# Performance work log

Measured on AMD Instinct MI355X. Metric: run time of the kernel, lower is better.

The kernel has to match this reference:

```python
import jax, jax.numpy as jnp
import numpy as np

V = 32000      # vocab
TMAX = 1024    # BLOCK_SIZE
D = 768        # N_EMBD
H = 12         # N_HEAD
L = 12         # N_LAYER
HS = D // H    # head_size
FF = 4 * D
B, T = 4, 1024


def setup_inputs() -> dict:
    key = jax.random.key(0)
    ks = iter(jax.random.split(key, 40))
    n = lambda shape: 0.02 * jax.random.normal(next(ks), shape, dtype=jnp.float32)
    return dict(
        idx=jax.random.randint(next(ks), (B, T), 0, V),
        targets=jax.random.randint(next(ks), (B, T), 0, V),
        tok_emb=n((V, D)),
        pos_emb=n((TMAX, D)),
        Wq=n((L, H, D, HS)), Wk=n((L, H, D, HS)), Wv=n((L, H, D, HS)),
        Wo=n((L, D, D)), bo=jnp.zeros((L, D)),
        W1=n((L, D, FF)), b1=jnp.zeros((L, FF)),
        W2=n((L, FF, D)), b2=jnp.zeros((L, D)),
        ln1_g=jnp.ones((L, D)), ln1_b=jnp.zeros((L, D)),
        ln2_g=jnp.ones((L, D)), ln2_b=jnp.zeros((L, D)),
        lnf_g=jnp.ones((D,)), lnf_b=jnp.zeros((D,)),
        Wlm=n((D, V)), blm=jnp.zeros((V,)),
    )


def _ln(x, g, b, eps=1e-5):
    m = x.mean(-1, keepdims=True)
    v = x.var(-1, keepdims=True)
    return (x - m) * jax.lax.rsqrt(v + eps) * g + b


def reference(idx, targets, tok_emb, pos_emb, Wq, Wk, Wv, Wo, bo,
              W1, b1, W2, b2, ln1_g, ln1_b, ln2_g, ln2_b, lnf_g, lnf_b,
              Wlm, blm):
    Bsz, Tt = idx.shape
    x = tok_emb[idx] + pos_emb[:Tt]                      # [B,T,D]
    causal = jnp.tril(jnp.ones((Tt, Tt), dtype=bool))     # [T,T]

    def layer(x, p):
        wq, wk, wv, wo, bob, w1, b1b, w2, b2b, g1, be1, g2, be2 = p
        h = _ln(x, g1, be1)
        q = jnp.einsum('btd,hdk->bhtk', h, wq)
        k = jnp.einsum('btd,hdk->bhtk', h, wk)
        v = jnp.einsum('btd,hdk->bhtk', h, wv)
        wei = jnp.einsum('bhtk,bhsk->bhts', q, k) * (HS ** -0.5)
        wei = jnp.where(causal, wei, -jnp.inf)
        wei = jax.nn.softmax(wei, axis=-1)                # dropout=0 in eval
        att = jnp.einsum('bhts,bhsk->bhtk', wei, v)
        att = att.transpose(0, 2, 1, 3).reshape(Bsz, Tt, H * HS)  # concat heads
        x = x + att @ wo + bob
        h2 = _ln(x, g2, be2)
        x = x + jax.nn.relu(h2 @ w1 + b1b) @ w2 + b2b
        return x, None

    x, _ = jax.lax.scan(layer, x,
                        (Wq, Wk, Wv, Wo, bo, W1, b1, W2, b2,
                         ln1_g, ln1_b, ln2_g, ln2_b))
    x = _ln(x, lnf_g, lnf_b)
    logits = x @ Wlm + blm                                # [B,T,V]
    lf = logits.reshape(Bsz * Tt, V)
    tf = targets.reshape(-1)
    logp = jax.nn.log_softmax(lf, axis=-1)
    loss = -jnp.take_along_axis(logp, tf[:, None], axis=1).mean()
    return lf, loss
```

## Files before the change

kernel.cpp:

```cpp
#include <hip/hip_runtime.h>

constexpr int C_B   = 4;
constexpr int C_T   = 1024;
constexpr int C_D   = 768;
constexpr int C_H   = 12;
constexpr int C_HS  = 64;
constexpr int C_FF  = 3072;
constexpr int C_V   = 32000;
constexpr int C_L   = 12;
constexpr int ROWS  = C_B * C_T;
constexpr int QKVN  = 3 * C_D;
constexpr int NCB   = C_V / 256;

typedef __bf16 bf16;
typedef __attribute__((ext_vector_type(8))) __bf16 bf16x8;
typedef __attribute__((ext_vector_type(4))) float  f32x4;
typedef __attribute__((ext_vector_type(4))) short  s16x4;

static __device__ __forceinline__ void gload16(const void* g, void* l) {
  __builtin_amdgcn_global_load_lds((const __attribute__((address_space(1))) void*)g,
                                   (__attribute__((address_space(3))) void*)l,
                                   16, 0, 0);
}

__global__ __launch_bounds__(256) void embed_kernel(const int* __restrict__ idx,
    const float* __restrict__ tok, const float* __restrict__ pos, float* __restrict__ x) {
  int gid = blockIdx.x * 256 + threadIdx.x;
  int row = gid / C_D, d = gid - row * C_D;
  int t = row & (C_T - 1);
  x[gid] = tok[(long)idx[row] * C_D + d] + pos[(long)t * C_D + d];
}

__global__ __launch_bounds__(256) void ln_kernel(const float* __restrict__ x,
    const float* __restrict__ g, const float* __restrict__ bb, long goff,
    bf16* __restrict__ out) {
  int row = blockIdx.x, tid = threadIdx.x;
  const float* xr = x + (long)row * C_D;
  float v0 = xr[tid], v1 = xr[tid + 256], v2 = xr[tid + 512];
  float s = v0 + v1 + v2;
  float s2 = v0 * v0 + v1 * v1 + v2 * v2;
#pragma unroll
  for (int off = 32; off > 0; off >>= 1) {
    s  += __shfl_down(s, off);
    s2 += __shfl_down(s2, off);
  }
  __shared__ float sm[4], sq[4];
  if ((tid & 63) == 0) { sm[tid >> 6] = s; sq[tid >> 6] = s2; }
  __syncthreads();
  s  = sm[0] + sm[1] + sm[2] + sm[3];
  s2 = sq[0] + sq[1] + sq[2] + sq[3];
  float mean = s * (1.f / C_D);
  float var  = s2 * (1.f / C_D) - mean * mean;
  float rstd = rsqrtf(var + 1e-5f);
  bf16* orow = out + (long)row * C_D;
  orow[tid]       = (bf16)((v0 - mean) * rstd * g[goff + tid]       + bb[goff + tid]);
  orow[tid + 256] = (bf16)((v1 - mean) * rstd * g[goff + tid + 256] + bb[goff + tid + 256]);
  orow[tid + 512] = (bf16)((v2 - mean) * rstd * g[goff + tid + 512] + bb[goff + tid + 512]);
}

__global__ __launch_bounds__(256) void transpose_all_kernel(
    const float* __restrict__ Wq, const float* __restrict__ Wk,
    const float* __restrict__ Wv, const float* __restrict__ Wo,
    const float* __restrict__ W1, const float* __restrict__ W2,
    const float* __restrict__ Wlm,
    bf16* __restrict__ wqkvt, bf16* __restrict__ wot,
    bf16* __restrict__ w1t, bf16* __restrict__ w2t, bf16* __restrict__ wlmt) {
  int bid = blockIdx.x;
  const float* src; bf16* dst; int K, N, ntn, t;
  if (bid < 82944) {
    int l = bid / 6912, sub = bid % 6912;
    if (sub < 1728) {
      int which = sub / 576, r = sub % 576, head = r / 48;
      t = r % 48;
      const float* W = which == 0 ? Wq : which == 1 ? Wk : Wv;
      src = W + (long)l * C_H * C_D * C_HS + (long)head * C_D * C_HS;
      dst = wqkvt + (long)l * QKVN * C_D + (long)which * C_D * C_D + (long)head * C_HS * C_D;
      K = C_D; N = C_HS; ntn = 2;
    } else if (sub < 2304) {
      t = sub - 1728;
      src = Wo + (long)l * C_D * C_D;  dst = wot + (long)l * C_D * C_D;
      K = C_D; N = C_D; ntn = 24;
    } else if (sub < 4608) {
      t = sub - 2304;
      src = W1 + (long)l * C_D * C_FF; dst = w1t + (long)l * C_FF * C_D;
      K = C_D; N = C_FF; ntn = 96;
    } else {
      t = sub - 4608;
      src = W2 + (long)l * C_FF * C_D; dst = w2t + (long)l * C_D * C_FF;
      K = C_FF; N = C_D; ntn = 24;
    }
  } else {
    t = bid - 82944; src = Wlm; dst = wlmt;
    K = C_D; N = C_V; ntn = C_V / 32;
  }
  __shared__ bf16 tile[32][33];
  int tn = t % ntn, tk = t / ntn;
  int c = threadIdx.x & 31, r = threadIdx.x >> 5;
#pragma unroll
  for (int it = 0; it < 4; ++it)
    tile[r + 8 * it][c] = (bf16)src[(long)(tk * 32 + r + 8 * it) * N + tn * 32 + c];
  __syncthreads();
#pragma unroll
  for (int it = 0; it < 4; ++it)
    dst[(long)(tn * 32 + r + 8 * it) * K + tk * 32 + c] = tile[c][r + 8 * it];
}

template <int MODE>
__global__ __launch_bounds__(512) void gemm256(const bf16* __restrict__ A,
    const bf16* __restrict__ Bt, const float* __restrict__ bias, long boff,
    void* __restrict__ outp, float* __restrict__ lossp, int N, int K) {
  __shared__ __attribute__((aligned(16))) char smem[131072];
  int tid = threadIdx.x;
  int l = tid & 63, w = tid >> 6;
  int wm = w >> 2, wn = w & 3;
  int lg = l >> 4, lr = l & 15;

  int nwg = gridDim.x;
  int fid = blockIdx.x;
  int swz = (fid & 7) * (nwg >> 3) + (fid >> 3);
  long row0 = (long)(swz & 15) * 256;
  long col0 = (long)(swz >> 4) * 256;
  int cbi = (int)(col0 >> 8);

  int Y0 = tid * 16, Y1 = 8192 + tid * 16;
  auto dec = [](int Y, int& R, int& C) {
    int s = Y >> 10, y = Y & 1023;
    int r15 = y >> 6, z = y & 63;
    int q = (z ^ ((r15 & 8) << 2)) >> 4;
    R = (s >> 1) * 16 + r15;
    C = (s & 1) * 32 + q * 8;
  };
  int R0, C0, R1, C1;
  dec(Y0, R0, C0);  dec(Y1, R1, C1);
  const bf16* Ab = A  + row0 * K;
  const bf16* Bb = Bt + col0 * K;

  auto stage = [&](int d, int kt) {
    char* bb = smem + d * 65536;
    long kc = (long)kt * 64;
    gload16(Ab + (long)R0 * K + kc + C0, bb + Y0);
    gload16(Ab + (long)R1 * K + kc + C1, bb + Y1);
    gload16(Ab + (long)(128 + R0) * K + kc + C0, bb + 16384 + Y0);
    gload16(Ab + (long)(128 + R1) * K + kc + C1, bb + 16384 + Y1);
    gload16(Bb + (long)R0 * K + kc + C0, bb + 32768 + Y0);
    gload16(Bb + (long)R1 * K + kc + C1, bb + 32768 + Y1);
    gload16(Bb + (long)(128 + R0) * K + kc + C0, bb + 49152 + Y0);
    gload16(Bb + (long)(128 + R1) * K + kc + C1, bb + 49152 + Y1);
  };

  f32x4 acc[8][4];
  const f32x4 fz = {0.f, 0.f, 0.f, 0.f};
#pragma unroll
  for (int mf = 0; mf < 8; ++mf)
#pragma unroll
    for (int nf = 0; nf < 4; ++nf) acc[mf][nf] = fz;

  int aoff = lr * 64 + ((lg * 16) ^ ((lr & 8) << 2));
  int nk = K >> 6;
  stage(0, 0);
  int d = 0;
  for (int kt = 0; kt < nk; ++kt) {
    __syncthreads();
    if (kt + 1 < nk) stage(d ^ 1, kt + 1);
    const char* aB = smem + d * 65536 + wm * 16384;
    const char* bB = smem + d * 65536 + 32768 + (wn >> 1) * 16384;
    bf16x8 bfrag[4][2];
#pragma unroll
    for (int nf = 0; nf < 4; ++nf)
#pragma unroll
      for (int k = 0; k < 2; ++k)
        bfrag[nf][k] = *(const bf16x8*)(bB + ((((wn & 1) * 4 + nf) * 2 + k) << 10) + aoff);
#pragma unroll
    for (int p = 0; p < 4; ++p) {
      bf16x8 af[2][2];
#pragma unroll
      for (int mi = 0; mi < 2; ++mi)
#pragma unroll
        for (int k = 0; k < 2; ++k)
          af[mi][k] = *(const bf16x8*)(aB + (((p * 2 + mi) * 2 + k) << 10) + aoff);
      __builtin_amdgcn_s_setprio(1);
#pragma unroll
      for (int mi = 0; mi < 2; ++mi)
#pragma unroll
        for (int nf = 0; nf < 4; ++nf)
#pragma unroll
          for (int k = 0; k < 2; ++k)
            acc[p * 2 + mi][nf] = __builtin_amdgcn_mfma_f32_16x16x32_bf16(
                af[mi][k], bfrag[nf][k], acc[p * 2 + mi][nf], 0, 0, 0);
      __builtin_amdgcn_s_setprio(0);
    }
    d ^= 1;
  }
  __syncthreads();

  if (MODE == 0 || MODE == 1) {
    bf16* lc = (bf16*)smem;
#pragma unroll
    for (int nf = 0; nf < 4; ++nf) {
      int col = wn * 64 + nf * 16 + lr;
      float bv = bias ? bias[boff + col0 + col] : 0.f;
#pragma unroll
      for (int mf = 0; mf < 8; ++mf) {
        int rb = wm * 128 + mf * 16 + lg * 4;
#pragma unroll
        for (int r = 0; r < 4; ++r) {
          float v = acc[mf][nf][r] + bv;
          if (MODE == 1) v = fmaxf(v, 0.f);
          lc[(rb + r) * 256 + col] = (bf16)v;
        }
      }
    }
    __syncthreads();
#pragma unroll
    for (int it = 0; it < 16; ++it) {
      int byte = it * 8192 + tid * 16;
      int rl = byte >> 9, cb = byte & 511;
      *(bf16x8*)((bf16*)outp + (row0 + rl) * N + col0 + (cb >> 1)) =
          *(const bf16x8*)(smem + byte);
    }
  } else {
#pragma unroll
    for (int h = 0; h < 2; ++h) {
      if (h) __syncthreads();
      if (wm == h) {
        float* lf = (float*)smem;
#pragma unroll
        for (int nf = 0; nf < 4; ++nf) {
          int col = wn * 64 + nf * 16 + lr;
          float bv = bias ? bias[boff + col0 + col] : 0.f;
#pragma unroll
          for (int mf = 0; mf < 8; ++mf) {
            int rb = mf * 16 + lg * 4;
#pragma unroll
            for (int r = 0; r < 4; ++r)
              lf[(rb + r) * 256 + col] = acc[mf][nf][r] + bv;
          }
        }
      }
      __syncthreads();
#pragma unroll
      for (int it = 0; it < 16; ++it) {
        int byte = it * 8192 + tid * 16;
        int rl = byte >> 10, cb = byte & 1023;
        *(f32x4*)((float*)outp + (row0 + h * 128 + rl) * N + col0 + (cb >> 2)) =
            *(const f32x4*)(smem + byte);
      }
      if (MODE == 3 && lossp) {
        const float* lf = (const float*)smem;
        int row = tid >> 2, chunk = tid & 3;
        float M = -1e30f, S = 0.f;
#pragma unroll
        for (int j = 0; j < 16; ++j) {
          int jj = (j + row) & 15;
          f32x4 v = *(const f32x4*)(lf + row * 256 + chunk * 64 + jj * 4);
#pragma unroll
          for (int q = 0; q < 4; ++q) {
            float xv = v[q];
            if (xv > M) { S *= __expf(M - xv); M = xv; }
            S += __expf(xv - M);
          }
        }
#pragma unroll
        for (int off = 1; off < 4; off <<= 1) {
          float Mo = __shfl_xor(M, off), So = __shfl_xor(S, off);
          float Mn = fmaxf(M, Mo);
          S = S * __expf(M - Mn) + So * __expf(Mo - Mn);
          M = Mn;
        }
        if (chunk == 0) {
          long pi = ((row0 + h * 128 + row) * NCB + cbi) * 2;
          lossp[pi] = M;  lossp[pi + 1] = S;
        }
      }
    }
  }
}

template <int MODE>
__global__ __launch_bounds__(256) void gemm_bt(const bf16* __restrict__ A,
    const bf16* __restrict__ Bt, const float* __restrict__ bias, long boff,
    void* __restrict__ outp, float* __restrict__ resid, int N, int K) {
  __shared__ __attribute__((aligned(16))) char smem[32768];
  int tid = threadIdx.x;
  int l = tid & 63;
  int w = tid >> 6, wr = w >> 1, wc = w & 1;
  int lg = l >> 4, lr = l & 15;

  int nwg = gridDim.x;
  int fid = blockIdx.x;
  int swz = (fid & 7) * (nwg >> 3) + (fid >> 3);
  long row0 = (long)(swz & 31) * 128;
  long col0 = (long)(swz >> 5) * 128;

  const bf16* ga = A  + (row0 + (tid >> 2)) * K + (tid & 3) * 8;
  const bf16* gb = Bt + (col0 + (tid >> 2)) * K + (tid & 3) * 8;

  f32x4 acc[4][4];
  const f32x4 fz = {0.f, 0.f, 0.f, 0.f};
#pragma unroll
  for (int m = 0; m < 4; ++m)
#pragma unroll
    for (int n = 0; n < 4; ++n) acc[m][n] = fz;

  int nk = K >> 5;
  {
    bf16* la = (bf16*)smem + tid * 8;
    bf16* lb = (bf16*)(smem + 8192) + tid * 8;
    gload16(ga, la);  gload16(ga + (long)64 * K, la + 2048);
    gload16(gb, lb);  gload16(gb + (long)64 * K, lb + 2048);
    ga += 32; gb += 32;
  }
  int cur = 0;
  for (int t = 0; t < nk; ++t) {
    __syncthreads();
    if (t + 1 < nk) {
      char* bufb = smem + (cur ^ 1) * 16384;
      bf16* la = (bf16*)bufb + tid * 8;
      bf16* lb = (bf16*)(bufb + 8192) + tid * 8;
      gload16(ga, la);  gload16(ga + (long)64 * K, la + 2048);
      gload16(gb, lb);  gload16(gb + (long)64 * K, lb + 2048);
      ga += 32; gb += 32;
    }
    const bf16* cA = (const bf16*)(smem + cur * 16384);
    const bf16* cB = (const bf16*)(smem + cur * 16384 + 8192);
    bf16x8 af[4], bfr[4];
#pragma unroll
    for (int m = 0; m < 4; ++m)
      af[m] = *(const bf16x8*)(cA + (wr * 64 + m * 16 + lr) * 32 + lg * 8);
#pragma unroll
    for (int n = 0; n < 4; ++n)
      bfr[n] = *(const bf16x8*)(cB + (wc * 64 + n * 16 + lr) * 32 + lg * 8);
#pragma unroll
    for (int m = 0; m < 4; ++m)
#pragma unroll
      for (int n = 0; n < 4; ++n)
        acc[m][n] = __builtin_amdgcn_mfma_f32_16x16x32_bf16(af[m], bfr[n], acc[m][n], 0, 0, 0);
    cur ^= 1;
  }
  __syncthreads();

  if (MODE == 0 || MODE == 1) {
    bf16* lc = (bf16*)smem;
#pragma unroll
    for (int n = 0; n < 4; ++n) {
      int gcl = wc * 64 + n * 16 + lr;
      float bv = bias ? bias[boff + col0 + gcl] : 0.f;
#pragma unroll
      for (int m = 0; m < 4; ++m) {
        int rb = wr * 64 + m * 16 + lg * 4;
#pragma unroll
        for (int r = 0; r < 4; ++r) {
          float v = acc[m][n][r] + bv;
          if (MODE == 1) v = fmaxf(v, 0.f);
          lc[(rb + r) * 128 + gcl] = (bf16)v;
        }
      }
    }
    __syncthreads();
#pragma unroll
    for (int it = 0; it < 8; ++it) {
      int byte = it * 4096 + tid * 16;
      int rl = byte >> 8;
      int cb = byte & 255;
      *(bf16x8*)((bf16*)outp + (row0 + rl) * N + col0 + (cb >> 1)) =
          *(const bf16x8*)(smem + byte);
    }
  } else {
#pragma unroll
    for (int pair = 0; pair < 2; ++pair) {
      float* lcf = (float*)smem;
#pragma unroll
      for (int n = 0; n < 4; ++n) {
        int gcl = wc * 64 + n * 16 + lr;
        float bv = bias ? bias[boff + col0 + gcl] : 0.f;
#pragma unroll
        for (int mi = 0; mi < 2; ++mi) {
          int m = pair * 2 + mi;
          int rl = wr * 32 + mi * 16 + lg * 4;
#pragma unroll
          for (int r = 0; r < 4; ++r)
            lcf[(rl + r) * 128 + gcl] = acc[m][n][r] + bv;
        }
      }
      __syncthreads();
#pragma unroll
      for (int it = 0; it < 8; ++it) {
        int byte = it * 4096 + tid * 16;
        int rl = byte >> 9;
        int cb = byte & 511;
        long gr = row0 + (rl >> 5) * 64 + pair * 32 + ((rl >> 4) & 1) * 16 + (rl & 15);
        f32x4 v = *(const f32x4*)(smem + byte);
        if (MODE == 2) {
          f32x4 g = *(const f32x4*)(resid + gr * N + col0 + (cb >> 2));
          v += g;
          *(f32x4*)(resid + gr * N + col0 + (cb >> 2)) = v;
        } else {
          *(f32x4*)((float*)outp + gr * N + col0 + (cb >> 2)) = v;
        }
      }
      __syncthreads();
    }
  }
}

#define TRRD(D, OFF) asm volatile("ds_read_b64_tr_b16 %0, %1 offset:" OFF \
                                  : "=v"(D) : "v"(trp))
__global__ __launch_bounds__(64) void attn_kernel(const bf16* __restrict__ qkv,
                                                  bf16* __restrict__ attout) {
  int fid = blockIdx.x;
  int swzb = (fid & 7) * 384 + (fid >> 3);
  int qt = swzb & 63;
  int bh = swzb >> 6;
  int b = bh / C_H, h = bh % C_H;
  int l = threadIdx.x;
  int lg = l >> 4, lr = l & 15;
  const bf16* base = qkv + (long)b * C_T * QKVN;

  const bf16* qp = base + (long)(qt * 16 + lr) * QKVN + h * C_HS;
  bf16x8 qf0 = *(const bf16x8*)(qp + lg * 8);
  bf16x8 qf1 = *(const bf16x8*)(qp + 32 + lg * 8);

  const f32x4 fz = {0.f, 0.f, 0.f, 0.f};
  f32x4 o[4] = {fz, fz, fz, fz};
  float m_run[4], l_run[4];
#pragma unroll
  for (int r = 0; r < 4; ++r) { m_run[r] = -1e30f; l_run[r] = 0.f; }

  __shared__ __attribute__((aligned(16))) bf16 p_lds[16][40];
  __shared__ __attribute__((aligned(16))) bf16 vt_sub[2048];

  unsigned trp = (unsigned)(unsigned long)
      ((const __attribute__((address_space(3))) char*)vt_sub + l * 8);

  int nkt = (qt * 16 + 15) / 32 + 1;
  for (int kt = 0; kt < nkt; ++kt) {
    int key0 = kt * 32;
    f32x4 sacc[2];
#pragma unroll
    for (int ss = 0; ss < 2; ++ss) {
      const bf16* kp = base + (long)(key0 + ss * 16 + lr) * QKVN + C_D + h * C_HS;
      bf16x8 kf0 = *(const bf16x8*)(kp + lg * 8);
      bf16x8 kf1 = *(const bf16x8*)(kp + 32 + lg * 8);
      f32x4 a = fz;
      a = __builtin_amdgcn_mfma_f32_16x16x32_bf16(qf0, kf0, a, 0, 0, 0);
      a = __builtin_amdgcn_mfma_f32_16x16x32_bf16(qf1, kf1, a, 0, 0, 0);
      sacc[ss] = a;
    }
#pragma unroll
    for (int r = 0; r < 4; ++r) {
      int qrow = qt * 16 + lg * 4 + r;
      bool u0 = (key0 + lr) <= qrow;
      bool u1 = (key0 + 16 + lr) <= qrow;
      float s0 = u0 ? sacc[0][r] * 0.125f : -1e30f;
      float s1 = u1 ? sacc[1][r] * 0.125f : -1e30f;
      float mr = fmaxf(s0, s1);
      mr = fmaxf(mr, __shfl_xor(mr, 1));
      mr = fmaxf(mr, __shfl_xor(mr, 2));
      mr = fmaxf(mr, __shfl_xor(mr, 4));
      mr = fmaxf(mr, __shfl_xor(mr, 8));
      float mnew = fmaxf(m_run[r], mr);
      float scale = __expf(m_run[r] - mnew);
      float p0 = u0 ? __expf(s0 - mnew) : 0.f;
      float p1 = u1 ? __expf(s1 - mnew) : 0.f;
      float rs = p0 + p1;
      rs += __shfl_xor(rs, 1);
      rs += __shfl_xor(rs, 2);
      rs += __shfl_xor(rs, 4);
      rs += __shfl_xor(rs, 8);
      l_run[r] = l_run[r] * scale + rs;
      m_run[r] = mnew;
      o[0][r] *= scale; o[1][r] *= scale; o[2][r] *= scale; o[3][r] *= scale;
      p_lds[lg * 4 + r][lr]      = (bf16)p0;
      p_lds[lg * 4 + r][16 + lr] = (bf16)p1;
    }
#pragma unroll
    for (int it = 0; it < 4; ++it) {
      int kl = it * 8 + (l >> 3);
      int d0 = (l & 7) * 8;
      bf16x8 vv = *(const bf16x8*)(base + (long)(key0 + kl) * QKVN + 2 * C_D + h * C_HS + d0);
      int ba = ((d0 >> 4) << 10) + (((kl >> 2) & 1) << 9) + ((kl >> 3) << 7)
             + ((kl & 3) << 5) + ((d0 & 15) << 1);
      *(bf16x8*)((char*)vt_sub + ba) = vv;
    }
    __syncthreads();
    s16x4 t0a, t0b, t1a, t1b, t2a, t2b, t3a, t3b;
    TRRD(t0a, "0");    TRRD(t0b, "512");
    TRRD(t1a, "1024"); TRRD(t1b, "1536");
    TRRD(t2a, "2048"); TRRD(t2b, "2560");
    TRRD(t3a, "3072"); TRRD(t3b, "3584");
    bf16x8 pf = *(const bf16x8*)(&p_lds[lr][lg * 8]);
    asm volatile("s_waitcnt lgkmcnt(0)" ::: "memory");
    __builtin_amdgcn_sched_barrier(0);
    union uu { short s[8]; bf16x8 v; };
    auto mk = [](s16x4 a, s16x4 bq) {
      uu u;
      u.s[0] = a[0]; u.s[1] = a[1]; u.s[2] = a[2]; u.s[3] = a[3];
      u.s[4] = bq[0]; u.s[5] = bq[1]; u.s[6] = bq[2]; u.s[7] = bq[3];
      return u.v;
    };
    o[0] = __builtin_amdgcn_mfma_f32_16x16x32_bf16(pf, mk(t0a, t0b), o[0], 0, 0, 0);
    o[1] = __builtin_amdgcn_mfma_f32_16x16x32_bf16(pf, mk(t1a, t1b), o[1], 0, 0, 0);
    o[2] = __builtin_amdgcn_mfma_f32_16x16x32_bf16(pf, mk(t2a, t2b), o[2], 0, 0, 0);
    o[3] = __builtin_amdgcn_mfma_f32_16x16x32_bf16(pf, mk(t3a, t3b), o[3], 0, 0, 0);
    __syncthreads();
  }
#pragma unroll
  for (int c = 0; c < 4; ++c)
#pragma unroll
    for (int r = 0; r < 4; ++r) {
      int qrow = qt * 16 + lg * 4 + r;
      attout[((long)b * C_T + qrow) * C_D + h * C_HS + c * 16 + lr] =
          (bf16)(o[c][r] / l_run[r]);
    }
}

__global__ __launch_bounds__(128) void loss_partial_kernel(const float* __restrict__ lossp,
    const float* __restrict__ logits, const int* __restrict__ targets,
    float* __restrict__ rowloss) {
  int row = blockIdx.x * 128 + threadIdx.x;
  const float* pp = lossp + (long)row * NCB * 2;
  float M = -1e30f, S = 0.f;
  for (int i = 0; i < NCB; ++i) {
    float pm = pp[i * 2], ps = pp[i * 2 + 1];
    float Mn = fmaxf(M, pm);
    S = S * __expf(M - Mn) + ps * __expf(pm - Mn);
    M = Mn;
  }
  float lt = logits[(long)row * C_V + targets[row]];
  rowloss[row] = -(lt - M - logf(S));
}

__global__ __launch_bounds__(256) void loss_final(const float* __restrict__ rowloss,
                                                  float* __restrict__ out) {
  int tid = threadIdx.x;
  float s = 0.f;
  for (int i = tid; i < ROWS; i += 256) s += rowloss[i];
#pragma unroll
  for (int off = 32; off > 0; off >>= 1) s += __shfl_down(s, off);
  __shared__ float sm[4];
  if ((tid & 63) == 0) sm[tid >> 6] = s;
  __syncthreads();
  if (tid == 0) out[0] = (sm[0] + sm[1] + sm[2] + sm[3]) * (1.f / ROWS);
}

extern "C" void kernel_launch(void* const* d_in, const int* in_sizes, int n_in,
                              void* d_out, int out_size, void* d_ws, size_t ws_size,
                              hipStream_t stream) {
  (void)in_sizes; (void)n_in; (void)out_size; (void)ws_size;
  const int*   idx     = (const int*)  d_in[0];
  const int*   targets = (const int*)  d_in[1];
  const float* tok     = (const float*)d_in[2];
  const float* pos     = (const float*)d_in[3];
  const float* Wq      = (const float*)d_in[4];
  const float* Wk      = (const float*)d_in[5];
  const float* Wv      = (const float*)d_in[6];
  const float* Wo      = (const float*)d_in[7];
  const float* bo      = (const float*)d_in[8];
  const float* W1      = (const float*)d_in[9];
  const float* b1      = (const float*)d_in[10];
  const float* W2      = (const float*)d_in[11];
  const float* b2      = (const float*)d_in[12];
  const float* ln1g    = (const float*)d_in[13];
  const float* ln1b    = (const float*)d_in[14];
  const float* ln2g    = (const float*)d_in[15];
  const float* ln2b    = (const float*)d_in[16];
  const float* lnfg    = (const float*)d_in[17];
  const float* lnfb    = (const float*)d_in[18];
  const float* Wlm     = (const float*)d_in[19];
  const float* blm     = (const float*)d_in[20];

  char* p = (char*)d_ws;
  auto alloc = [&](size_t bytes) {
    char* r = p; p += (bytes + 255) & ~(size_t)255; return r;
  };
  float* x       = (float*)alloc((size_t)ROWS * C_D * 4);
  bf16*  h       = (bf16*) alloc((size_t)ROWS * C_D * 2);
  bf16*  qkv     = (bf16*) alloc((size_t)ROWS * QKVN * 2);
  bf16*  attout  = (bf16*) alloc((size_t)ROWS * C_D * 2);
  bf16*  ffbuf   = (bf16*) alloc((size_t)ROWS * C_FF * 2);
  bf16*  wqkvt   = (bf16*) alloc((size_t)C_L * QKVN * C_D * 2);
  bf16*  wot     = (bf16*) alloc((size_t)C_L * C_D * C_D * 2);
  bf16*  w1t     = (bf16*) alloc((size_t)C_L * C_FF * C_D * 2);
  bf16*  w2t     = (bf16*) alloc((size_t)C_L * C_D * C_FF * 2);
  bf16*  wlmt    = (bf16*) alloc((size_t)C_V * C_D * 2);
  float* rowloss = (float*)alloc((size_t)ROWS * 4);
  float* lossp   = (float*)alloc((size_t)ROWS * NCB * 2 * 4);

  float* logits = (float*)d_out;

  transpose_all_kernel<<<106944, 256, 0, stream>>>(
      Wq, Wk, Wv, Wo, W1, W2, Wlm, wqkvt, wot, w1t, w2t, wlmt);
  embed_kernel<<<ROWS * C_D / 256, 256, 0, stream>>>(idx, tok, pos, x);

  for (int l = 0; l < C_L; ++l) {
    ln_kernel<<<ROWS, 256, 0, stream>>>(x, ln1g, ln1b, (long)l * C_D, h);
    gemm_bt<0><<<(QKVN / 128) * 32, 256, 0, stream>>>(
        h, wqkvt + (long)l * QKVN * C_D, nullptr, 0, qkv, nullptr, QKVN, C_D);
    attn_kernel<<<C_B * C_H * (C_T / 16), 64, 0, stream>>>(qkv, attout);
    gemm_bt<2><<<(C_D / 128) * 32, 256, 0, stream>>>(
        attout, wot + (long)l * C_D * C_D, bo, (long)l * C_D, nullptr, x, C_D, C_D);
    ln_kernel<<<ROWS, 256, 0, stream>>>(x, ln2g, ln2b, (long)l * C_D, h);
    gemm_bt<1><<<(C_FF / 128) * 32, 256, 0, stream>>>(
        h, w1t + (long)l * C_FF * C_D, b1, (long)l * C_FF, ffbuf, nullptr, C_FF, C_D);
    gemm_bt<2><<<(C_D / 128) * 32, 256, 0, stream>>>(
        ffbuf, w2t + (long)l * C_D * C_FF, b2, (long)l * C_D, nullptr, x, C_D, C_FF);
  }

  ln_kernel<<<ROWS, 256, 0, stream>>>(x, lnfg, lnfb, 0, h);
  gemm256<3><<<16 * (C_V / 256), 512, 0, stream>>>(
      h, wlmt, blm, 0, logits, lossp, C_V, C_D);
  loss_partial_kernel<<<ROWS / 128, 128, 0, stream>>>(lossp, logits, targets, rowloss);
  loss_final<<<1, 256, 0, stream>>>(rowloss, logits + (long)ROWS * C_V);
}
```

Baseline: 3.262 ms.

## Transpose weights per layer into reused buffers and widen attention key tiles

Weight transposition now runs per layer into single-layer buffers, and the LM-head weight transpose reuses the qkv buffer after the layer loop, which shrinks the workspace footprint. The attention kernel processes 64 keys per iteration instead of 32, halving loop trips and syncs at the cost of more registers and LDS. Dead MODE branches in the GEMM epilogues are removed. The per-layer transposes add kernel launches and serialize weight conversion between layers.

```diff
diff --git a/kernel.cpp b/kernel.cpp
--- a/kernel.cpp
+++ b/kernel.cpp
@@ -58,40 +58,45 @@
   orow[tid + 512] = (bf16)((v2 - mean) * rstd * g[goff + tid + 512] + bb[goff + tid + 512]);
 }
 
-__global__ __launch_bounds__(256) void transpose_all_kernel(
+__global__ __launch_bounds__(256) void transpose_kernel(const float* __restrict__ src,
+    bf16* __restrict__ dst, int K, int N, long soff0, int ntn) {
+  __shared__ bf16 tile[32][33];
+  const float* s = src + soff0;
+  int tn = blockIdx.x % ntn, tk = blockIdx.x / ntn;
+  int c = threadIdx.x & 31, r = threadIdx.x >> 5;
+#pragma unroll
+  for (int it = 0; it < 4; ++it)
+    tile[r + 8 * it][c] = (bf16)s[(long)(tk * 32 + r + 8 * it) * N + tn * 32 + c];
+  __syncthreads();
+#pragma unroll
+  for (int it = 0; it < 4; ++it)
+    dst[(long)(tn * 32 + r + 8 * it) * K + tk * 32 + c] = tile[c][r + 8 * it];
+}
+
+__global__ __launch_bounds__(256) void transpose_layer_kernel(
     const float* __restrict__ Wq, const float* __restrict__ Wk,
     const float* __restrict__ Wv, const float* __restrict__ Wo,
     const float* __restrict__ W1, const float* __restrict__ W2,
-    const float* __restrict__ Wlm,
     bf16* __restrict__ wqkvt, bf16* __restrict__ wot,
-    bf16* __restrict__ w1t, bf16* __restrict__ w2t, bf16* __restrict__ wlmt) {
+    bf16* __restrict__ w1t, bf16* __restrict__ w2t, int l) {
   int bid = blockIdx.x;
   const float* src; bf16* dst; int K, N, ntn, t;
-  if (bid < 82944) {
-    int l = bid / 6912, sub = bid % 6912;
-    if (sub < 1728) {
-      int which = sub / 576, r = sub % 576, head = r / 48;
-      t = r % 48;
-      const float* W = which == 0 ? Wq : which == 1 ? Wk : Wv;
-      src = W + (long)l * C_H * C_D * C_HS + (long)head * C_D * C_HS;
-      dst = wqkvt + (long)l * QKVN * C_D + (long)which * C_D * C_D + (long)head * C_HS * C_D;
-      K = C_D; N = C_HS; ntn = 2;
-    } else if (sub < 2304) {
-      t = sub - 1728;
-      src = Wo + (long)l * C_D * C_D;  dst = wot + (long)l * C_D * C_D;
-      K = C_D; N = C_D; ntn = 24;
-    } else if (sub < 4608) {
-      t = sub - 2304;
-      src = W1 + (long)l * C_D * C_FF; dst = w1t + (long)l * C_FF * C_D;
-      K = C_D; N = C_FF; ntn = 96;
-    } else {
-      t = sub - 4608;
-      src = W2 + (long)l * C_FF * C_D; dst = w2t + (long)l * C_D * C_FF;
-      K = C_FF; N = C_D; ntn = 24;
-    }
+  if (bid < 1728) {
+    int which = bid / 576, r = bid % 576, head = r / 48;
+    t = r % 48;
+    const float* W = which == 0 ? Wq : which == 1 ? Wk : Wv;
+    src = W + (long)l * C_H * C_D * C_HS + (long)head * C_D * C_HS;
+    dst = wqkvt + (long)which * C_D * C_D + (long)head * C_HS * C_D;
+    K = C_D; N = C_HS; ntn = 2;
+  } else if (bid < 2304) {
+    t = bid - 1728; src = Wo + (long)l * C_D * C_D; dst = wot;
+    K = C_D; N = C_D; ntn = 24;
+  } else if (bid < 4608) {
+    t = bid - 2304; src = W1 + (long)l * C_D * C_FF; dst = w1t;
+    K = C_D; N = C_FF; ntn = 96;
   } else {
-    t = bid - 82944; src = Wlm; dst = wlmt;
-    K = C_D; N = C_V; ntn = C_V / 32;
+    t = bid - 4608; src = W2 + (long)l * C_FF * C_D; dst = w2t;
+    K = C_FF; N = C_D; ntn = 24;
   }
   __shared__ bf16 tile[32][33];
   int tn = t % ntn, tk = t / ntn;
@@ -193,20 +198,21 @@
   }
   __syncthreads();
 
-  if (MODE == 0 || MODE == 1) {
-    bf16* lc = (bf16*)smem;
-#pragma unroll
-    for (int nf = 0; nf < 4; ++nf) {
-      int col = wn * 64 + nf * 16 + lr;
-      float bv = bias ? bias[boff + col0 + col] : 0.f;
-#pragma unroll
-      for (int mf = 0; mf < 8; ++mf) {
-        int rb = wm * 128 + mf * 16 + lg * 4;
-#pragma unroll
-        for (int r = 0; r < 4; ++r) {
-          float v = acc[mf][nf][r] + bv;
-          if (MODE == 1) v = fmaxf(v, 0.f);
-          lc[(rb + r) * 256 + col] = (bf16)v;
+#pragma unroll
+  for (int h = 0; h < 2; ++h) {
+    if (h) __syncthreads();
+    if (wm == h) {
+      float* lf = (float*)smem;
+#pragma unroll
+      for (int nf = 0; nf < 4; ++nf) {
+        int col = wn * 64 + nf * 16 + lr;
+        float bv = bias ? bias[boff + col0 + col] : 0.f;
+#pragma unroll
+        for (int mf = 0; mf < 8; ++mf) {
+          int rb = mf * 16 + lg * 4;
+#pragma unroll
+          for (int r = 0; r < 4; ++r)
+            lf[(rb + r) * 256 + col] = acc[mf][nf][r] + bv;
         }
       }
     }
@@ -214,63 +220,35 @@
 #pragma unroll
     for (int it = 0; it < 16; ++it) {
       int byte = it * 8192 + tid * 16;
-      int rl = byte >> 9, cb = byte & 511;
-      *(bf16x8*)((bf16*)outp + (row0 + rl) * N + col0 + (cb >> 1)) =
-          *(const bf16x8*)(smem + byte);
-    }
-  } else {
-#pragma unroll
-    for (int h = 0; h < 2; ++h) {
-      if (h) __syncthreads();
-      if (wm == h) {
-        float* lf = (float*)smem;
-#pragma unroll
-        for (int nf = 0; nf < 4; ++nf) {
-          int col = wn * 64 + nf * 16 + lr;
-          float bv = bias ? bias[boff + col0 + col] : 0.f;
-#pragma unroll
-          for (int mf = 0; mf < 8; ++mf) {
-            int rb = mf * 16 + lg * 4;
-#pragma unroll
-            for (int r = 0; r < 4; ++r)
-              lf[(rb + r) * 256 + col] = acc[mf][nf][r] + bv;
-          }
+      int rl = byte >> 10, cb = byte & 1023;
+      *(f32x4*)((float*)outp + (row0 + h * 128 + rl) * N + col0 + (cb >> 2)) =
+          *(const f32x4*)(smem + byte);
+    }
+    if (lossp) {
+      const float* lf = (const float*)smem;
+      int row = tid >> 2, chunk = tid & 3;
+      float M = -1e30f, S = 0.f;
+#pragma unroll
+      for (int j = 0; j < 16; ++j) {
+        int jj = (j + row) & 15;
+        f32x4 v = *(const f32x4*)(lf + row * 256 + chunk * 64 + jj * 4);
+#pragma unroll
+        for (int q = 0; q < 4; ++q) {
+          float xv = v[q];
+          if (xv > M) { S *= __expf(M - xv); M = xv; }
+          S += __expf(xv - M);
         }
       }
-      __syncthreads();
-#pragma unroll
-      for (int it = 0; it < 16; ++it) {
-        int byte = it * 8192 + tid * 16;
-        int rl = byte >> 10, cb = byte & 1023;
-        *(f32x4*)((float*)outp + (row0 + h * 128 + rl) * N + col0 + (cb >> 2)) =
-            *(const f32x4*)(smem + byte);
-      }
-      if (MODE == 3 && lossp) {
-        const float* lf = (const float*)smem;
-        int row = tid >> 2, chunk = tid & 3;
-        float M = -1e30f, S = 0.f;
-#pragma unroll
-        for (int j = 0; j < 16; ++j) {
-          int jj = (j + row) & 15;
-          f32x4 v = *(const f32x4*)(lf + row * 256 + chunk * 64 + jj * 4);
-#pragma unroll
-          for (int q = 0; q < 4; ++q) {
-            float xv = v[q];
-            if (xv > M) { S *= __expf(M - xv); M = xv; }
-            S += __expf(xv - M);
-          }
-        }
-#pragma unroll
-        for (int off = 1; off < 4; off <<= 1) {
-          float Mo = __shfl_xor(M, off), So = __shfl_xor(S, off);
-          float Mn = fmaxf(M, Mo);
-          S = S * __expf(M - Mn) + So * __expf(Mo - Mn);
-          M = Mn;
-        }
-        if (chunk == 0) {
-          long pi = ((row0 + h * 128 + row) * NCB + cbi) * 2;
-          lossp[pi] = M;  lossp[pi + 1] = S;
-        }
+#pragma unroll
+      for (int off = 1; off < 4; off <<= 1) {
+        float Mo = __shfl_xor(M, off), So = __shfl_xor(S, off);
+        float Mn = fmaxf(M, Mo);
+        S = S * __expf(M - Mn) + So * __expf(Mo - Mn);
+        M = Mn;
+      }
+      if (chunk == 0) {
+        long pi = ((row0 + h * 128 + row) * NCB + cbi) * 2;
+        lossp[pi] = M;  lossp[pi + 1] = S;
       }
     }
   }
@@ -390,13 +368,9 @@
         int cb = byte & 511;
         long gr = row0 + (rl >> 5) * 64 + pair * 32 + ((rl >> 4) & 1) * 16 + (rl & 15);
         f32x4 v = *(const f32x4*)(smem + byte);
-        if (MODE == 2) {
-          f32x4 g = *(const f32x4*)(resid + gr * N + col0 + (cb >> 2));
-          v += g;
-          *(f32x4*)(resid + gr * N + col0 + (cb >> 2)) = v;
-        } else {
-          *(f32x4*)((float*)outp + gr * N + col0 + (cb >> 2)) = v;
-        }
+        f32x4 g = *(const f32x4*)(resid + gr * N + col0 + (cb >> 2));
+        v += g;
+        *(f32x4*)(resid + gr * N + col0 + (cb >> 2)) = v;
       }
       __syncthreads();
     }
@@ -426,18 +400,18 @@
 #pragma unroll
   for (int r = 0; r < 4; ++r) { m_run[r] = -1e30f; l_run[r] = 0.f; }
 
-  __shared__ __attribute__((aligned(16))) bf16 p_lds[16][40];
-  __shared__ __attribute__((aligned(16))) bf16 vt_sub[2048];
+  __shared__ __attribute__((aligned(16))) bf16 p_lds[16][80];
+  __shared__ __attribute__((aligned(16))) bf16 vt_sub[4096];
 
   unsigned trp = (unsigned)(unsigned long)
       ((const __attribute__((address_space(3))) char*)vt_sub + l * 8);
 
-  int nkt = (qt * 16 + 15) / 32 + 1;
+  int nkt = (qt * 16 + 15) / 64 + 1;
   for (int kt = 0; kt < nkt; ++kt) {
-    int key0 = kt * 32;
-    f32x4 sacc[2];
-#pragma unroll
-    for (int ss = 0; ss < 2; ++ss) {
+    int key0 = kt * 64;
+    f32x4 sacc[4];
+#pragma unroll
+    for (int ss = 0; ss < 4; ++ss) {
       const bf16* kp = base + (long)(key0 + ss * 16 + lr) * QKVN + C_D + h * C_HS;
       bf16x8 kf0 = *(const bf16x8*)(kp + lg * 8);
       bf16x8 kf1 = *(const bf16x8*)(kp + 32 + lg * 8);
@@ -449,20 +423,25 @@
 #pragma unroll
     for (int r = 0; r < 4; ++r) {
       int qrow = qt * 16 + lg * 4 + r;
-      bool u0 = (key0 + lr) <= qrow;
-      bool u1 = (key0 + 16 + lr) <= qrow;
-      float s0 = u0 ? sacc[0][r] * 0.125f : -1e30f;
-      float s1 = u1 ? sacc[1][r] * 0.125f : -1e30f;
-      float mr = fmaxf(s0, s1);
+      float sv[4];
+#pragma unroll
+      for (int ss = 0; ss < 4; ++ss) {
+        bool u = (key0 + ss * 16 + lr) <= qrow;
+        sv[ss] = u ? sacc[ss][r] * 0.125f : -1e30f;
+      }
+      float mr = fmaxf(fmaxf(sv[0], sv[1]), fmaxf(sv[2], sv[3]));
       mr = fmaxf(mr, __shfl_xor(mr, 1));
       mr = fmaxf(mr, __shfl_xor(mr, 2));
       mr = fmaxf(mr, __shfl_xor(mr, 4));
       mr = fmaxf(mr, __shfl_xor(mr, 8));
       float mnew = fmaxf(m_run[r], mr);
       float scale = __expf(m_run[r] - mnew);
-      float p0 = u0 ? __expf(s0 - mnew) : 0.f;
-      float p1 = u1 ? __expf(s1 - mnew) : 0.f;
-      float rs = p0 + p1;
+      float pv[4], rs = 0.f;
+#pragma unroll
+      for (int ss = 0; ss < 4; ++ss) {
+        pv[ss] = sv[ss] > -1e29f ? __expf(sv[ss] - mnew) : 0.f;
+        rs += pv[ss];
+      }
       rs += __shfl_xor(rs, 1);
       rs += __shfl_xor(rs, 2);
       rs += __shfl_xor(rs, 4);
@@ -470,25 +449,32 @@
       l_run[r] = l_run[r] * scale + rs;
       m_run[r] = mnew;
       o[0][r] *= scale; o[1][r] *= scale; o[2][r] *= scale; o[3][r] *= scale;
-      p_lds[lg * 4 + r][lr]      = (bf16)p0;
-      p_lds[lg * 4 + r][16 + lr] = (bf16)p1;
-    }
-#pragma unroll
-    for (int it = 0; it < 4; ++it) {
+#pragma unroll
+      for (int ss = 0; ss < 4; ++ss)
+        p_lds[lg * 4 + r][ss * 16 + lr] = (bf16)pv[ss];
+    }
+#pragma unroll
+    for (int it = 0; it < 8; ++it) {
       int kl = it * 8 + (l >> 3);
       int d0 = (l & 7) * 8;
       bf16x8 vv = *(const bf16x8*)(base + (long)(key0 + kl) * QKVN + 2 * C_D + h * C_HS + d0);
-      int ba = ((d0 >> 4) << 10) + (((kl >> 2) & 1) << 9) + ((kl >> 3) << 7)
-             + ((kl & 3) << 5) + ((d0 & 15) << 1);
+      int klh = kl & 31;
+      int ba = ((kl >> 5) << 12) + ((d0 >> 4) << 10) + (((klh >> 2) & 1) << 9)
+             + ((klh >> 3) << 7) + ((klh & 3) << 5) + ((d0 & 15) << 1);
       *(bf16x8*)((char*)vt_sub + ba) = vv;
     }
     __syncthreads();
-    s16x4 t0a, t0b, t1a, t1b, t2a, t2b, t3a, t3b;
-    TRRD(t0a, "0");    TRRD(t0b, "512");
-    TRRD(t1a, "1024"); TRRD(t1b, "1536");
-    TRRD(t2a, "2048"); TRRD(t2b, "2560");
-    TRRD(t3a, "3072"); TRRD(t3b, "3584");
-    bf16x8 pf = *(const bf16x8*)(&p_lds[lr][lg * 8]);
+    s16x4 h0[8], h1[8];
+    TRRD(h0[0], "0");    TRRD(h0[1], "512");
+    TRRD(h0[2], "1024"); TRRD(h0[3], "1536");
+    TRRD(h0[4], "2048"); TRRD(h0[5], "2560");
+    TRRD(h0[6], "3072"); TRRD(h0[7], "3584");
+    TRRD(h1[0], "4096"); TRRD(h1[1], "4608");
+    TRRD(h1[2], "5120"); TRRD(h1[3], "5632");
+    TRRD(h1[4], "6144"); TRRD(h1[5], "6656");
+    TRRD(h1[6], "7168"); TRRD(h1[7], "7680");
+    bf16x8 pf0 = *(const bf16x8*)(&p_lds[lr][lg * 8]);
+    bf16x8 pf1 = *(const bf16x8*)(&p_lds[lr][32 + lg * 8]);
     asm volatile("s_waitcnt lgkmcnt(0)" ::: "memory");
     __builtin_amdgcn_sched_barrier(0);
     union uu { short s[8]; bf16x8 v; };
@@ -498,10 +484,11 @@
       u.s[4] = bq[0]; u.s[5] = bq[1]; u.s[6] = bq[2]; u.s[7] = bq[3];
       return u.v;
     };
-    o[0] = __builtin_amdgcn_mfma_f32_16x16x32_bf16(pf, mk(t0a, t0b), o[0], 0, 0, 0);
-    o[1] = __builtin_amdgcn_mfma_f32_16x16x32_bf16(pf, mk(t1a, t1b), o[1], 0, 0, 0);
-    o[2] = __builtin_amdgcn_mfma_f32_16x16x32_bf16(pf, mk(t2a, t2b), o[2], 0, 0, 0);
-    o[3] = __builtin_amdgcn_mfma_f32_16x16x32_bf16(pf, mk(t3a, t3b), o[3], 0, 0, 0);
+#pragma unroll
+    for (int c = 0; c < 4; ++c) {
+      o[c] = __builtin_amdgcn_mfma_f32_16x16x32_bf16(pf0, mk(h0[c*2], h0[c*2+1]), o[c], 0, 0, 0);
+      o[c] = __builtin_amdgcn_mfma_f32_16x16x32_bf16(pf1, mk(h1[c*2], h1[c*2+1]), o[c], 0, 0, 0);
+    }
     __syncthreads();
   }
 #pragma unroll
@@ -578,33 +565,37 @@
   bf16*  qkv     = (bf16*) alloc((size_t)ROWS * QKVN * 2);
   bf16*  attout  = (bf16*) alloc((size_t)ROWS * C_D * 2);
   bf16*  ffbuf   = (bf16*) alloc((size_t)ROWS * C_FF * 2);
-  bf16*  wqkvt   = (bf16*) alloc((size_t)C_L * QKVN * C_D * 2);
-  bf16*  wot     = (bf16*) alloc((size_t)C_L * C_D * C_D * 2);
-  bf16*  w1t     = (bf16*) alloc((size_t)C_L * C_FF * C_D * 2);
-  bf16*  w2t     = (bf16*) alloc((size_t)C_L * C_D * C_FF * 2);
-  bf16*  wlmt    = (bf16*) alloc((size_t)C_V * C_D * 2);
+  bf16*  wqkvt   = (bf16*) alloc((size_t)QKVN * C_D * 2);
+  bf16*  wot     = (bf16*) alloc((size_t)C_D * C_D * 2);
+  bf16*  w1t     = (bf16*) alloc((size_t)C_FF * C_D * 2);
+  bf16*  w2t     = (bf16*) alloc((size_t)C_D * C_FF * 2);
   float* rowloss = (float*)alloc((size_t)ROWS * 4);
   float* lossp   = (float*)alloc((size_t)ROWS * NCB * 2 * 4);
+  bf16*  wlmt    = qkv;
 
   float* logits = (float*)d_out;
 
-  transpose_all_kernel<<<106944, 256, 0, stream>>>(
-      Wq, Wk, Wv, Wo, W1, W2, Wlm, wqkvt, wot, w1t, w2t, wlmt);
   embed_kernel<<<ROWS * C_D / 256, 256, 0, stream>>>(idx, tok, pos, x);
 
   for (int l = 0; l < C_L; ++l) {
+    transpose_layer_kernel<<<6912, 256, 0, stream>>>(
+        Wq, Wk, Wv, Wo, W1, W2, wqkvt, wot, w1t, w2t, l);
+
     ln_kernel<<<ROWS, 256, 0, stream>>>(x, ln1g, ln1b, (long)l * C_D, h);
     gemm_bt<0><<<(QKVN / 128) * 32, 256, 0, stream>>>(
-        h, wqkvt + (long)l * QKVN * C_D, nullptr, 0, qkv, nullptr, QKVN, C_D);
+        h, wqkvt, nullptr, 0, qkv, nullptr, QKVN, C_D);
     attn_kernel<<<C_B * C_H * (C_T / 16), 64, 0, stream>>>(qkv, attout);
     gemm_bt<2><<<(C_D / 128) * 32, 256, 0, stream>>>(
-        attout, wot + (long)l * C_D * C_D, bo, (long)l * C_D, nullptr, x, C_D, C_D);
+        attout, wot, bo, (long)l * C_D, nullptr, x, C_D, C_D);
     ln_kernel<<<ROWS, 256, 0, stream>>>(x, ln2g, ln2b, (long)l * C_D, h);
     gemm_bt<1><<<(C_FF / 128) * 32, 256, 0, stream>>>(
-        h, w1t + (long)l * C_FF * C_D, b1, (long)l * C_FF, ffbuf, nullptr, C_FF, C_D);
+        h, w1t, b1, (long)l * C_FF, ffbuf, nullptr, C_FF, C_D);
     gemm_bt<2><<<(C_D / 128) * 32, 256, 0, stream>>>(
-        ffbuf, w2t + (long)l * C_D * C_FF, b2, (long)l * C_D, nullptr, x, C_D, C_FF);
-  }
+        ffbuf, w2t, b2, (long)l * C_D, nullptr, x, C_D, C_FF);
+  }
+
+  transpose_kernel<<<(C_V / 32) * (C_D / 32), 256, 0, stream>>>(
+      Wlm, wlmt, C_D, C_V, 0, C_V / 32);
 
   ln_kernel<<<ROWS, 256, 0, stream>>>(x, lnfg, lnfb, 0, h);
   gemm256<3><<<16 * (C_V / 256), 512, 0, stream>>>(
```

Result: no change. 3.243 ms (-0.6%).
